# Optimization experiments

Hardware: AMD Instinct MI355X
Metric: run time of the kernel (lower is better)

## Reference

```python
import jax, jax.numpy as jnp
import numpy as np

EMBED = 256
HID = EMBED * 4
NUM_EXPERTS = 4
WINDOW = 16
B, T = 4, 4096
EPS = 1e-5


def _ln(x, g, b):
    m = jnp.mean(x, axis=-1, keepdims=True)
    v = jnp.mean(jnp.square(x - m), axis=-1, keepdims=True)
    return (x - m) / jnp.sqrt(v + EPS) * g + b


def setup_inputs() -> dict:
    key = jax.random.key(0)
    ks = jax.random.split(key, 16)
    s = 0.02
    d = {
        'x': jax.random.normal(ks[0], (B, T, EMBED), jnp.float32),
        'ln1_g': jnp.ones((EMBED,), jnp.float32),
        'ln1_b': jnp.zeros((EMBED,), jnp.float32),
        'qkv_w': jax.random.normal(ks[1], (EMBED, 3 * EMBED), jnp.float32) * s,
        'qkv_b': jnp.zeros((3 * EMBED,), jnp.float32),
        'proj_w': jax.random.normal(ks[2], (EMBED, EMBED), jnp.float32) * s,
        'proj_b': jnp.zeros((EMBED,), jnp.float32),
        'attn_gate': jnp.ones((EMBED,), jnp.float32),
        'ln2_g': jnp.ones((EMBED,), jnp.float32),
        'ln2_b': jnp.zeros((EMBED,), jnp.float32),
        'gating_w': jax.random.normal(ks[3], (EMBED, NUM_EXPERTS), jnp.float32) * s,
        'gating_b': jnp.zeros((NUM_EXPERTS,), jnp.float32),
        'e_w1': jax.random.normal(ks[4], (NUM_EXPERTS, EMBED, HID), jnp.float32) * s,
        'e_b1': jnp.zeros((NUM_EXPERTS, HID), jnp.float32),
        'e_w2': jax.random.normal(ks[5], (NUM_EXPERTS, HID, EMBED), jnp.float32) * s,
        'e_b2': jnp.zeros((NUM_EXPERTS, EMBED), jnp.float32),
    }
    return d


def reference(x, ln1_g, ln1_b, qkv_w, qkv_b, proj_w, proj_b, attn_gate,
              ln2_g, ln2_b, gating_w, gating_b, e_w1, e_b1, e_w2, e_b2):
    Bx, Tx, C = x.shape
    # --- sparse attention branch ---
    h = _ln(x, ln1_g, ln1_b)
    qkv = h @ qkv_w + qkv_b                      # [B,T,3C]
    q, k, v = jnp.split(qkv, 3, axis=-1)
    scores = jnp.einsum('btc,bsc->bts', q, k) / jnp.sqrt(jnp.float32(C))
    idx = jnp.arange(Tx)
    diff = idx[:, None] - idx[None, :]           # i - j
    in_window = (diff >= 0) & (diff <= WINDOW)
    # faithful to torch code: scores outside the window (but causal) stay 0,
    # positions above the diagonal become -inf; softmax over full row
    scores = jnp.where(in_window, scores, 0.0)
    scores = jnp.where(diff >= 0, scores, -jnp.inf)
    att = jax.nn.softmax(scores, axis=-1)        # [B,T,T]
    a_out = jnp.einsum('bts,bsc->btc', att, v) * attn_gate
    x = x + a_out @ proj_w + proj_b
    # --- dense all-expert MoE branch ---
    h2 = _ln(x, ln2_g, ln2_b)
    gates = jax.nn.softmax(h2 @ gating_w + gating_b, axis=-1)     # [B,T,E]
    hid = jax.nn.gelu(jnp.einsum('btc,ech->bteh', h2, e_w1) + e_b1,
                      approximate=False)                           # [B,T,E,H]
    eo = jnp.einsum('bteh,eho->bteo', hid, e_w2) + e_b2            # [B,T,E,C]
    moe_out = jnp.einsum('bte,bteo->bto', gates, eo)
    return x + moe_out
```

## Files before the change

### kernel.cpp

```cpp
#include <hip/hip_runtime.h>
#include <hip/hip_bf16.h>
#include <math.h>

#define T_   4096
#define B_   4
#define C_   256
#define C3_  768
#define H_   1024
#define E_   4
#define M_   (B_*T_)
#define NCH_ 64
#define CHL_ (T_/NCH_)

typedef __attribute__((ext_vector_type(8))) short short8;
typedef __attribute__((ext_vector_type(4))) float floatx4;

__device__ __forceinline__ float b2f(unsigned short u) {
  union { unsigned int i; float f; } x; x.i = ((unsigned int)u) << 16; return x.f;
}
__device__ __forceinline__ unsigned short f2b(float f) {
  __hip_bfloat16 h = __float2bfloat16(f);
  return *reinterpret_cast<unsigned short*>(&h);
}
__device__ __forceinline__ void unpack8(uint4 a, float* f) {
  unsigned int w[4] = {a.x, a.y, a.z, a.w};
  #pragma unroll
  for (int i = 0; i < 4; i++) {
    union { unsigned int u; float g; } lo, hi;
    lo.u = w[i] << 16; hi.u = w[i] & 0xffff0000u;
    f[2*i] = lo.g; f[2*i+1] = hi.g;
  }
}
__device__ __forceinline__ void gl_lds16(const unsigned short* g, unsigned short* l) {
  __builtin_amdgcn_global_load_lds(
      (const __attribute__((address_space(1))) void*)g,
      (__attribute__((address_space(3))) void*)l, 16, 0, 0);
}
__device__ __forceinline__ float gelu_f(float v) {
  float s = v * 0.70710678118f;
  float a = fabsf(s);
  float t = __builtin_amdgcn_rcpf(1.0f + 0.47047f * a);
  float poly = t * (0.3480242f + t * (-0.0958798f + t * 0.7478556f));
  float e = __expf(-a * a);
  float erfa = 1.0f - poly * e;
  float erfv = (s >= 0.f) ? erfa : -erfa;
  return 0.5f * v * (1.0f + erfv);
}

__global__ __launch_bounds__(256) void transpose_cvt(
    const float* __restrict__ src, unsigned short* __restrict__ dst, int K, int N,
    int dstLd, size_t dstZStride) {
  __shared__ float tile[32][33];
  src += (size_t)blockIdx.z * K * N;
  dst += (size_t)blockIdx.z * dstZStride;
  int n0 = blockIdx.x * 32, k0 = blockIdx.y * 32;
  int tx = threadIdx.x, ty = threadIdx.y;
  #pragma unroll
  for (int i = 0; i < 32; i += 8)
    tile[ty + i][tx] = src[(size_t)(k0 + ty + i) * N + n0 + tx];
  __syncthreads();
  #pragma unroll
  for (int i = 0; i < 32; i += 8)
    dst[(size_t)(n0 + ty + i) * dstLd + k0 + tx] = f2b(tile[tx][ty + i]);
}

__global__ __launch_bounds__(256) void ln1_kernel(
    const float* __restrict__ x, const float* __restrict__ g,
    const float* __restrict__ b, unsigned short* __restrict__ h) {
  __shared__ float red[4];
  int row = blockIdx.x, tid = threadIdx.x;
  float v = x[(size_t)row * C_ + tid];
  float s = v;
  #pragma unroll
  for (int o = 32; o; o >>= 1) s += __shfl_xor(s, o);
  if ((tid & 63) == 0) red[tid >> 6] = s;
  __syncthreads();
  float mean = (red[0] + red[1] + red[2] + red[3]) * (1.0f / C_);
  __syncthreads();
  float d = v - mean;
  float q = d * d;
  #pragma unroll
  for (int o = 32; o; o >>= 1) q += __shfl_xor(q, o);
  if ((tid & 63) == 0) red[tid >> 6] = q;
  __syncthreads();
  float var = (red[0] + red[1] + red[2] + red[3]) * (1.0f / C_);
  h[(size_t)row * C_ + tid] = f2b(d * rsqrtf(var + 1e-5f) * g[tid] + b[tid]);
}

__global__ __launch_bounds__(256) void ln2_gates_kernel(
    const float* __restrict__ x1, const float* __restrict__ g,
    const float* __restrict__ b, const float* __restrict__ gw,
    const float* __restrict__ gb, unsigned short* __restrict__ h2,
    float* __restrict__ gates) {
  __shared__ float red[4];
  __shared__ float redg[4][4];
  int row = blockIdx.x, tid = threadIdx.x;
  float v = x1[(size_t)row * C_ + tid];
  float s = v;
  #pragma unroll
  for (int o = 32; o; o >>= 1) s += __shfl_xor(s, o);
  if ((tid & 63) == 0) red[tid >> 6] = s;
  __syncthreads();
  float mean = (red[0] + red[1] + red[2] + red[3]) * (1.0f / C_);
  __syncthreads();
  float d = v - mean;
  float q = d * d;
  #pragma unroll
  for (int o = 32; o; o >>= 1) q += __shfl_xor(q, o);
  if ((tid & 63) == 0) red[tid >> 6] = q;
  __syncthreads();
  float var = (red[0] + red[1] + red[2] + red[3]) * (1.0f / C_);
  float hv = d * rsqrtf(var + 1e-5f) * g[tid] + b[tid];
  h2[(size_t)row * C_ + tid] = f2b(hv);
  float p0 = hv * gw[tid * 4 + 0];
  float p1 = hv * gw[tid * 4 + 1];
  float p2 = hv * gw[tid * 4 + 2];
  float p3 = hv * gw[tid * 4 + 3];
  #pragma unroll
  for (int o = 32; o; o >>= 1) {
    p0 += __shfl_xor(p0, o); p1 += __shfl_xor(p1, o);
    p2 += __shfl_xor(p2, o); p3 += __shfl_xor(p3, o);
  }
  if ((tid & 63) == 0) {
    int w = tid >> 6;
    redg[w][0] = p0; redg[w][1] = p1; redg[w][2] = p2; redg[w][3] = p3;
  }
  __syncthreads();
  if (tid == 0) {
    float t4[4];
    #pragma unroll
    for (int e = 0; e < 4; e++)
      t4[e] = redg[0][e] + redg[1][e] + redg[2][e] + redg[3][e] + gb[e];
    float m = fmaxf(fmaxf(t4[0], t4[1]), fmaxf(t4[2], t4[3]));
    float zs = 0.f;
    #pragma unroll
    for (int e = 0; e < 4; e++) { t4[e] = __expf(t4[e] - m); zs += t4[e]; }
    float inv = 1.0f / zs;
    #pragma unroll
    for (int e = 0; e < 4; e++) gates[(size_t)row * 4 + e] = t4[e] * inv;
  }
}

__global__ __launch_bounds__(256) void scan1_kernel(const unsigned short* __restrict__ qkv,
                                                    float* __restrict__ S) {
  int b = blockIdx.x >> 6, ch = blockIdx.x & 63, c = threadIdx.x;
  float s = 0.f;
  size_t base = ((size_t)b * T_ + (size_t)ch * CHL_) * C3_ + 512 + c;
  for (int t = 0; t < CHL_; t++) s += b2f(qkv[base + (size_t)t * C3_]);
  S[((size_t)b * NCH_ + ch) * C_ + c] = s;
}
__global__ __launch_bounds__(256) void scan2_kernel(float* __restrict__ S) {
  int b = blockIdx.x, c = threadIdx.x;
  float run = 0.f;
  for (int ch = 0; ch < NCH_; ch++) {
    size_t i = ((size_t)b * NCH_ + ch) * C_ + c;
    float t = S[i]; S[i] = run; run += t;
  }
}
__global__ __launch_bounds__(256) void scan3_kernel(const unsigned short* __restrict__ qkv,
                                                    const float* __restrict__ S,
                                                    unsigned short* __restrict__ Pb) {
  int b = blockIdx.x >> 6, ch = blockIdx.x & 63, c = threadIdx.x;
  float run = S[((size_t)b * NCH_ + ch) * C_ + c];
  size_t row0 = (size_t)b * T_ + (size_t)ch * CHL_;
  for (int t = 0; t < CHL_; t++) {
    run += b2f(qkv[(row0 + t) * C3_ + 512 + c]);
    Pb[(row0 + t) * C_ + c] = f2b(run);
  }
}

__global__ __launch_bounds__(256) void attn_kernel(
    const unsigned short* __restrict__ qkv, const unsigned short* __restrict__ Pb,
    const float* __restrict__ gate, unsigned short* __restrict__ aout) {
  int wave = threadIdx.x >> 6, lane = threadIdx.x & 63;
  int r = blockIdx.x * 4 + wave;
  int t = r & (T_ - 1);
  int g = lane >> 4, u = lane & 15;
  const unsigned short* qp = qkv + (size_t)r * C3_ + (u << 4);
  float qv[16];
  unpack8(*(const uint4*)qp, qv);
  unpack8(*(const uint4*)(qp + 8), qv + 8);
  float sc[5];
  #pragma unroll
  for (int rnd = 0; rnd < 5; rnd++) {
    int j = rnd * 4 + g;
    int jj = t - 16 + j;
    bool valid = (j <= 16) && (jj >= 0);
    float d = 0.f;
    if (valid) {
      const unsigned short* kp = qkv + (size_t)(r - 16 + j) * C3_ + 256 + (u << 4);
      float kv[16];
      unpack8(*(const uint4*)kp, kv);
      unpack8(*(const uint4*)(kp + 8), kv + 8);
      #pragma unroll
      for (int c = 0; c < 16; c++) d += qv[c] * kv[c];
    }
    d += __shfl_xor(d, 1); d += __shfl_xor(d, 2);
    d += __shfl_xor(d, 4); d += __shfl_xor(d, 8);
    sc[rnd] = valid ? d * 0.0625f : -1e30f;
  }
  float m = fmaxf(fmaxf(fmaxf(sc[0], sc[1]), fmaxf(sc[2], sc[3])), sc[4]);
  m = fmaxf(m, __shfl_xor(m, 16));
  m = fmaxf(m, __shfl_xor(m, 32));
  if (t > 16) m = fmaxf(m, 0.0f);
  float ev[5], Zp = 0.f;
  #pragma unroll
  for (int rnd = 0; rnd < 5; rnd++) {
    ev[rnd] = (sc[rnd] > -1e29f) ? __expf(sc[rnd] - m) : 0.f;
    Zp += ev[rnd];
  }
  Zp += __shfl_xor(Zp, 16);
  Zp += __shfl_xor(Zp, 32);
  float e0v = 0.f;
  if (t > 16) { e0v = __expf(-m); Zp += e0v * (float)(t - 16); }
  float vp[16];
  #pragma unroll
  for (int c = 0; c < 16; c++) vp[c] = 0.f;
  #pragma unroll
  for (int rnd = 0; rnd < 5; rnd++) {
    if (ev[rnd] != 0.f) {
      int j = rnd * 4 + g;
      const unsigned short* vpp = qkv + (size_t)(r - 16 + j) * C3_ + 512 + (u << 4);
      float vv[16];
      unpack8(*(const uint4*)vpp, vv);
      unpack8(*(const uint4*)(vpp + 8), vv + 8);
      #pragma unroll
      for (int c = 0; c < 16; c++) vp[c] += ev[rnd] * vv[c];
    }
  }
  #pragma unroll
  for (int c = 0; c < 16; c++) {
    vp[c] += __shfl_xor(vp[c], 16);
    vp[c] += __shfl_xor(vp[c], 32);
  }
  if (g == 0) {
    if (t > 16) {
      const unsigned short* pp = Pb + (size_t)(r - 17) * C_ + (u << 4);
      float pv[16];
      unpack8(*(const uint4*)pp, pv);
      unpack8(*(const uint4*)(pp + 8), pv + 8);
      #pragma unroll
      for (int c = 0; c < 16; c++) vp[c] += e0v * pv[c];
    }
    float inv = 1.0f / Zp;
    const float* gp = gate + (u << 4);
    unsigned int ow[8];
    #pragma unroll
    for (int i = 0; i < 8; i++) {
      unsigned short lo = f2b(vp[2*i] * inv * gp[2*i]);
      unsigned short hi = f2b(vp[2*i+1] * inv * gp[2*i+1]);
      ow[i] = (unsigned int)lo | ((unsigned int)hi << 16);
    }
    uint4 s0 = {ow[0], ow[1], ow[2], ow[3]};
    uint4 s1 = {ow[4], ow[5], ow[6], ow[7]};
    *(uint4*)(aout + (size_t)r * C_ + (u << 4)) = s0;
    *(uint4*)(aout + (size_t)r * C_ + (u << 4) + 8) = s1;
  }
}

template<int EPI>
__global__ __launch_bounds__(256) void gemm128(
    const unsigned short* __restrict__ A, const unsigned short* __restrict__ Bt,
    const float* __restrict__ bias, int K, int ldOut,
    const float* __restrict__ resid, float* __restrict__ outf,
    unsigned short* __restrict__ outb, const float* __restrict__ gates) {
  __shared__ __align__(16) unsigned short As[128 * 64];
  __shared__ __align__(16) unsigned short Bs[128 * 64];
  const int tid = threadIdx.x;
  const int wave = tid >> 6, lane = tid & 63;
  const int mBlk = blockIdx.x * 128, nBlk = blockIdx.y * 128;
  const int wm = (wave >> 1) * 64, wn = (wave & 1) * 64;
  const int lm = lane & 15, lk = (lane >> 4) * 8;
  floatx4 acc[4][4];
  #pragma unroll
  for (int i = 0; i < 4; i++)
    #pragma unroll
    for (int j = 0; j < 4; j++) acc[i][j] = (floatx4){0.f, 0.f, 0.f, 0.f};

  for (int kt = 0; kt < K; kt += 64) {
    __syncthreads();
    #pragma unroll
    for (int i = 0; i < 4; i++) {
      int seg = i * 256 + tid;
      int row = seg >> 3, g = seg & 7;
      int gc = (g ^ (row & 7)) << 3;
      gl_lds16(A + (size_t)(mBlk + row) * K + kt + gc, &As[seg * 8]);
      gl_lds16(Bt + (size_t)(nBlk + row) * K + kt + gc, &Bs[seg * 8]);
    }
    __syncthreads();
    #pragma unroll
    for (int kk = 0; kk < 64; kk += 32) {
      short8 mf[4], nf[4];
      #pragma unroll
      for (int j = 0; j < 4; j++) {
        int row = wm + j * 16 + lm;
        mf[j] = *(const short8*)&As[row * 64 + ((((kk + lk) >> 3) ^ (row & 7)) << 3)];
      }
      #pragma unroll
      for (int i = 0; i < 4; i++) {
        int row = wn + i * 16 + lm;
        nf[i] = *(const short8*)&Bs[row * 64 + ((((kk + lk) >> 3) ^ (row & 7)) << 3)];
      }
      #pragma unroll
      for (int i = 0; i < 4; i++)
        #pragma unroll
        for (int j = 0; j < 4; j++)
          acc[i][j] = __builtin_amdgcn_mfma_f32_16x16x32_bf16(nf[i], mf[j], acc[i][j], 0, 0, 0);
    }
  }
  const int lc = lane & 15, q4 = (lane >> 4) * 4;
  const int eIdx = (EPI == 2) ? (nBlk >> 10) : 0;
  #pragma unroll
  for (int i = 0; i < 4; i++) {
    int n0 = nBlk + wn + i * 16 + q4;
    float4 bs = *(const float4*)&bias[n0];
    #pragma unroll
    for (int j = 0; j < 4; j++) {
      int m = mBlk + wm + j * 16 + lc;
      float v0 = acc[i][j][0] + bs.x, v1 = acc[i][j][1] + bs.y;
      float v2 = acc[i][j][2] + bs.z, v3 = acc[i][j][3] + bs.w;
      if (EPI == 0) {
        ushort4 o = {f2b(v0), f2b(v1), f2b(v2), f2b(v3)};
        *(ushort4*)&outb[(size_t)m * ldOut + n0] = o;
      } else if (EPI == 1) {
        size_t idx = (size_t)m * ldOut + n0;
        float4 r = *(const float4*)&resid[idx];
        float4 o = {v0 + r.x, v1 + r.y, v2 + r.z, v3 + r.w};
        *(float4*)&outf[idx] = o;
      } else {
        float g = gates[(size_t)m * E_ + eIdx];
        ushort4 o = {f2b(g * gelu_f(v0)), f2b(g * gelu_f(v1)),
                     f2b(g * gelu_f(v2)), f2b(g * gelu_f(v3))};
        *(ushort4*)&outb[(size_t)m * ldOut + n0] = o;
      }
    }
  }
}

__global__ __launch_bounds__(256) void gemm_down(
    const unsigned short* __restrict__ hid, const unsigned short* __restrict__ w2cat,
    const float* __restrict__ b2, const float* __restrict__ gates,
    const float* __restrict__ x1, float* __restrict__ out) {
  __shared__ __align__(16) unsigned short As[128 * 64];
  __shared__ __align__(16) unsigned short Bs[64 * 64];
  const int tid = threadIdx.x;
  const int wave = tid >> 6, lane = tid & 63;
  const int mBlk = blockIdx.x * 128, nBlk = blockIdx.y * 64;
  const int wm = wave * 32;
  const int lm = lane & 15, lk = (lane >> 4) * 8;
  floatx4 acc[4][2];
  #pragma unroll
  for (int i = 0; i < 4; i++)
    #pragma unroll
    for (int j = 0; j < 2; j++) acc[i][j] = (floatx4){0.f, 0.f, 0.f, 0.f};

  const int K = E_ * H_;
  for (int kt = 0; kt < K; kt += 64) {
    __syncthreads();
    #pragma unroll
    for (int i = 0; i < 4; i++) {
      int seg = i * 256 + tid;
      int row = seg >> 3, g = seg & 7;
      int gc = (g ^ (row & 7)) << 3;
      gl_lds16(hid + (size_t)(mBlk + row) * K + kt + gc, &As[seg * 8]);
    }
    #pragma unroll
    for (int i = 0; i < 2; i++) {
      int seg = i * 256 + tid;
      int row = seg >> 3, g = seg & 7;
      int gc = (g ^ (row & 7)) << 3;
      gl_lds16(w2cat + (size_t)(nBlk + row) * K + kt + gc, &Bs[seg * 8]);
    }
    __syncthreads();
    #pragma unroll
    for (int kk = 0; kk < 64; kk += 32) {
      short8 mf[2], nf[4];
      #pragma unroll
      for (int j = 0; j < 2; j++) {
        int row = wm + j * 16 + lm;
        mf[j] = *(const short8*)&As[row * 64 + ((((kk + lk) >> 3) ^ (row & 7)) << 3)];
      }
      #pragma unroll
      for (int i = 0; i < 4; i++) {
        int row = i * 16 + lm;
        nf[i] = *(const short8*)&Bs[row * 64 + ((((kk + lk) >> 3) ^ (row & 7)) << 3)];
      }
      #pragma unroll
      for (int i = 0; i < 4; i++)
        #pragma unroll
        for (int j = 0; j < 2; j++)
          acc[i][j] = __builtin_amdgcn_mfma_f32_16x16x32_bf16(nf[i], mf[j], acc[i][j], 0, 0, 0);
    }
  }
  const int lc = lane & 15, q4 = (lane >> 4) * 4;
  #pragma unroll
  for (int j = 0; j < 2; j++) {
    int m = mBlk + wm + j * 16 + lc;
    float4 g4 = *(const float4*)(gates + (size_t)m * 4);
    #pragma unroll
    for (int i = 0; i < 4; i++) {
      int n0 = nBlk + i * 16 + q4;
      float4 bA = *(const float4*)&b2[0 * C_ + n0];
      float4 bB = *(const float4*)&b2[1 * C_ + n0];
      float4 bC = *(const float4*)&b2[2 * C_ + n0];
      float4 bD = *(const float4*)&b2[3 * C_ + n0];
      size_t idx = (size_t)m * C_ + n0;
      float4 r = *(const float4*)&x1[idx];
      float4 o;
      o.x = acc[i][j][0] + r.x + g4.x*bA.x + g4.y*bB.x + g4.z*bC.x + g4.w*bD.x;
      o.y = acc[i][j][1] + r.y + g4.x*bA.y + g4.y*bB.y + g4.z*bC.y + g4.w*bD.y;
      o.z = acc[i][j][2] + r.z + g4.x*bA.z + g4.y*bB.z + g4.z*bC.z + g4.w*bD.z;
      o.w = acc[i][j][3] + r.w + g4.x*bA.w + g4.y*bB.w + g4.z*bC.w + g4.w*bD.w;
      *(float4*)&out[idx] = o;
    }
  }
}

extern "C" void kernel_launch(void* const* d_in, const int* in_sizes, int n_in,
                              void* d_out, int out_size, void* d_ws, size_t ws_size,
                              hipStream_t stream) {
  const float* x       = (const float*)d_in[0];
  const float* ln1_g   = (const float*)d_in[1];
  const float* ln1_b   = (const float*)d_in[2];
  const float* qkv_w   = (const float*)d_in[3];
  const float* qkv_b   = (const float*)d_in[4];
  const float* proj_w  = (const float*)d_in[5];
  const float* proj_b  = (const float*)d_in[6];
  const float* attn_g  = (const float*)d_in[7];
  const float* ln2_g   = (const float*)d_in[8];
  const float* ln2_b   = (const float*)d_in[9];
  const float* gat_w   = (const float*)d_in[10];
  const float* gat_b   = (const float*)d_in[11];
  const float* e_w1    = (const float*)d_in[12];
  const float* e_b1    = (const float*)d_in[13];
  const float* e_w2    = (const float*)d_in[14];
  const float* e_b2    = (const float*)d_in[15];
  float* out = (float*)d_out;

  char* p = (char*)d_ws;
  unsigned short* h    = (unsigned short*)p; p += (size_t)M_ * C_ * 2;
  unsigned short* qkv  = (unsigned short*)p; p += (size_t)M_ * C3_ * 2;
  unsigned short* Pb   = (unsigned short*)p; p += (size_t)M_ * C_ * 2;
  unsigned short* aout = (unsigned short*)p; p += (size_t)M_ * C_ * 2;
  float*          x1   = (float*)p;          p += (size_t)M_ * C_ * 4;
  unsigned short* h2   = (unsigned short*)p; p += (size_t)M_ * C_ * 2;
  float*          gts  = (float*)p;          p += (size_t)M_ * E_ * 4;
  float*          S    = (float*)p;          p += (size_t)B_ * NCH_ * C_ * 4;
  unsigned short* wq   = (unsigned short*)p; p += (size_t)C3_ * C_ * 2;
  unsigned short* wp   = (unsigned short*)p; p += (size_t)C_ * C_ * 2;
  unsigned short* w1t  = (unsigned short*)p; p += (size_t)E_ * H_ * C_ * 2;
  unsigned short* w2t  = (unsigned short*)p; p += (size_t)E_ * C_ * H_ * 2;
  unsigned short* hid  = (unsigned short*)p; p += (size_t)M_ * E_ * H_ * 2;

  dim3 t32x8(32, 8);
  transpose_cvt<<<dim3(C3_/32, C_/32, 1), t32x8, 0, stream>>>(qkv_w, wq, C_, C3_, C_, 0);
  transpose_cvt<<<dim3(C_/32, C_/32, 1),  t32x8, 0, stream>>>(proj_w, wp, C_, C_, C_, 0);
  transpose_cvt<<<dim3(H_/32, C_/32, E_), t32x8, 0, stream>>>(e_w1, w1t, C_, H_, C_, (size_t)H_ * C_);
  transpose_cvt<<<dim3(C_/32, H_/32, E_), t32x8, 0, stream>>>(e_w2, w2t, H_, C_, E_ * H_, (size_t)H_);

  ln1_kernel<<<M_, 256, 0, stream>>>(x, ln1_g, ln1_b, h);
  gemm128<0><<<dim3(M_/128, C3_/128), 256, 0, stream>>>(h, wq, qkv_b, C_, C3_,
      nullptr, nullptr, qkv, nullptr);
  scan1_kernel<<<B_*NCH_, 256, 0, stream>>>(qkv, S);
  scan2_kernel<<<B_, 256, 0, stream>>>(S);
  scan3_kernel<<<B_*NCH_, 256, 0, stream>>>(qkv, S, Pb);
  attn_kernel<<<M_/4, 256, 0, stream>>>(qkv, Pb, attn_g, aout);
  gemm128<1><<<dim3(M_/128, C_/128), 256, 0, stream>>>(aout, wp, proj_b, C_, C_,
      x, x1, nullptr, nullptr);
  ln2_gates_kernel<<<M_, 256, 0, stream>>>(x1, ln2_g, ln2_b, gat_w, gat_b, h2, gts);
  gemm128<2><<<dim3(M_/128, (E_*H_)/128), 256, 0, stream>>>(h2, w1t, e_b1, C_, E_ * H_,
      nullptr, nullptr, hid, gts);
  gemm_down<<<dim3(M_/128, C_/64), 256, 0, stream>>>(hid, w2t, e_b2, gts, x1, out);
}
```

Baseline: 373.6 us.

## Fuse MoE up and down projections into one kernel with split-expert partials

```diff
diff --git a/kernel.cpp b/kernel.cpp
--- a/kernel.cpp
+++ b/kernel.cpp
@@ -263,7 +263,7 @@
     const unsigned short* __restrict__ A, const unsigned short* __restrict__ Bt,
     const float* __restrict__ bias, int K, int ldOut,
     const float* __restrict__ resid, float* __restrict__ outf,
-    unsigned short* __restrict__ outb, const float* __restrict__ gates) {
+    unsigned short* __restrict__ outb) {
   __shared__ __align__(16) unsigned short As[128 * 64];
   __shared__ __align__(16) unsigned short Bs[128 * 64];
   const int tid = threadIdx.x;
@@ -309,7 +309,6 @@
     }
   }
   const int lc = lane & 15, q4 = (lane >> 4) * 4;
-  const int eIdx = (EPI == 2) ? (nBlk >> 10) : 0;
   #pragma unroll
   for (int i = 0; i < 4; i++) {
     int n0 = nBlk + wn + i * 16 + q4;
@@ -322,98 +321,140 @@
       if (EPI == 0) {
         ushort4 o = {f2b(v0), f2b(v1), f2b(v2), f2b(v3)};
         *(ushort4*)&outb[(size_t)m * ldOut + n0] = o;
-      } else if (EPI == 1) {
+      } else {
         size_t idx = (size_t)m * ldOut + n0;
         float4 r = *(const float4*)&resid[idx];
         float4 o = {v0 + r.x, v1 + r.y, v2 + r.z, v3 + r.w};
         *(float4*)&outf[idx] = o;
-      } else {
-        float g = gates[(size_t)m * E_ + eIdx];
-        ushort4 o = {f2b(g * gelu_f(v0)), f2b(g * gelu_f(v1)),
-                     f2b(g * gelu_f(v2)), f2b(g * gelu_f(v3))};
-        *(ushort4*)&outb[(size_t)m * ldOut + n0] = o;
       }
     }
   }
 }
 
-__global__ __launch_bounds__(256) void gemm_down(
-    const unsigned short* __restrict__ hid, const unsigned short* __restrict__ w2cat,
+__global__ __launch_bounds__(512, 2) void moe_fused(
+    const unsigned short* __restrict__ h2, const unsigned short* __restrict__ w1t,
+    const unsigned short* __restrict__ w2cat, const float* __restrict__ b1,
     const float* __restrict__ b2, const float* __restrict__ gates,
-    const float* __restrict__ x1, float* __restrict__ out) {
-  __shared__ __align__(16) unsigned short As[128 * 64];
-  __shared__ __align__(16) unsigned short Bs[64 * 64];
-  const int tid = threadIdx.x;
-  const int wave = tid >> 6, lane = tid & 63;
-  const int mBlk = blockIdx.x * 128, nBlk = blockIdx.y * 64;
-  const int wm = wave * 32;
-  const int lm = lane & 15, lk = (lane >> 4) * 8;
-  floatx4 acc[4][2];
+    const float* __restrict__ x1, float* __restrict__ part) {
+  __shared__ __align__(16) unsigned short w1b[2][32 * 256];
+  __shared__ __align__(16) unsigned short Pl[128 * 40];
+  const int tid = threadIdx.x, wave = tid >> 6, lane = tid & 63;
+  const int lm = lane & 15, quad = lane >> 4, q4 = quad * 4, lk = quad * 8;
+  const int mBlk = blockIdx.x * 128;
+  const int z = blockIdx.y, e0 = z * 2;
+  const int wm = (wave >> 2) * 64, wn = (wave & 3) * 64;
+  const int m1 = wave * 16 + lm;
+
+  const float g1a = gates[(size_t)(mBlk + m1) * 4 + e0];
+  const float g1b = gates[(size_t)(mBlk + m1) * 4 + e0 + 1];
+
+  short8 acache[8];
+  #pragma unroll
+  for (int ks = 0; ks < 8; ks++)
+    acache[ks] = *(const short8*)(h2 + (size_t)(mBlk + m1) * C_ + ks * 32 + lk);
+
+  floatx4 oacc[4][4];
   #pragma unroll
   for (int i = 0; i < 4; i++)
     #pragma unroll
-    for (int j = 0; j < 2; j++) acc[i][j] = (floatx4){0.f, 0.f, 0.f, 0.f};
-
-  const int K = E_ * H_;
-  for (int kt = 0; kt < K; kt += 64) {
+    for (int j = 0; j < 4; j++) oacc[i][j] = (floatx4){0.f, 0.f, 0.f, 0.f};
+
+  auto stage = [&](int ch, int buf) {
+    int e = e0 + (ch >> 5), hc = (ch & 31) * 32;
+    const unsigned short* w1src = w1t + ((size_t)e * H_ + hc) * C_;
+    #pragma unroll
+    for (int i = 0; i < 2; i++) {
+      int seg = i * 512 + tid;
+      int row = seg >> 5, s = seg & 31;
+      int sp = (s & 24) | ((s & 7) ^ (row & 7));
+      gl_lds16(w1src + (size_t)row * C_ + sp * 8, &w1b[buf][seg * 8]);
+    }
+  };
+
+  stage(0, 0);
+  __syncthreads();
+
+  #pragma unroll 1
+  for (int ch = 0; ch < 64; ch++) {
+    const int buf = ch & 1;
+    const int e = e0 + (ch >> 5), hc = (ch & 31) * 32;
+    short8 w2f[4];
+    #pragma unroll
+    for (int i = 0; i < 4; i++)
+      w2f[i] = *(const short8*)(w2cat + (size_t)(wn + i * 16 + lm) * (E_ * H_) +
+                                (size_t)e * H_ + hc + lk);
+    if (ch + 1 < 64) stage(ch + 1, buf ^ 1);
+    floatx4 pacc[2];
+    pacc[0] = (floatx4){0.f, 0.f, 0.f, 0.f};
+    pacc[1] = (floatx4){0.f, 0.f, 0.f, 0.f};
+    #pragma unroll
+    for (int ks = 0; ks < 8; ks++) {
+      int s = ks * 4 + quad;
+      #pragma unroll
+      for (int j = 0; j < 2; j++) {
+        int row = j * 16 + lm;
+        int sp = (s & 24) | ((s & 7) ^ (row & 7));
+        short8 nf = *(const short8*)&w1b[buf][row * 256 + sp * 8];
+        pacc[j] = __builtin_amdgcn_mfma_f32_16x16x32_bf16(nf, acache[ks], pacc[j], 0, 0, 0);
+      }
+    }
     __syncthreads();
+    const float ge = (ch >> 5) ? g1b : g1a;
+    #pragma unroll
+    for (int j = 0; j < 2; j++) {
+      float4 bb = *(const float4*)&b1[(size_t)e * H_ + hc + j * 16 + q4];
+      ushort4 o;
+      o.x = f2b(ge * gelu_f(pacc[j][0] + bb.x));
+      o.y = f2b(ge * gelu_f(pacc[j][1] + bb.y));
+      o.z = f2b(ge * gelu_f(pacc[j][2] + bb.z));
+      o.w = f2b(ge * gelu_f(pacc[j][3] + bb.w));
+      *(ushort4*)&Pl[m1 * 40 + j * 16 + q4] = o;
+    }
+    __syncthreads();
+    short8 mf[4];
+    #pragma unroll
+    for (int j = 0; j < 4; j++)
+      mf[j] = *(const short8*)&Pl[(wm + j * 16 + lm) * 40 + lk];
+    #pragma unroll
+    for (int i = 0; i < 4; i++)
+      #pragma unroll
+      for (int j = 0; j < 4; j++)
+        oacc[i][j] = __builtin_amdgcn_mfma_f32_16x16x32_bf16(w2f[i], mf[j], oacc[i][j], 0, 0, 0);
+  }
+  #pragma unroll
+  for (int j = 0; j < 4; j++) {
+    int m = mBlk + wm + j * 16 + lm;
+    float ga = gates[(size_t)m * 4 + e0];
+    float gb = gates[(size_t)m * 4 + e0 + 1];
     #pragma unroll
     for (int i = 0; i < 4; i++) {
-      int seg = i * 256 + tid;
-      int row = seg >> 3, g = seg & 7;
-      int gc = (g ^ (row & 7)) << 3;
-      gl_lds16(hid + (size_t)(mBlk + row) * K + kt + gc, &As[seg * 8]);
-    }
-    #pragma unroll
-    for (int i = 0; i < 2; i++) {
-      int seg = i * 256 + tid;
-      int row = seg >> 3, g = seg & 7;
-      int gc = (g ^ (row & 7)) << 3;
-      gl_lds16(w2cat + (size_t)(nBlk + row) * K + kt + gc, &Bs[seg * 8]);
-    }
-    __syncthreads();
-    #pragma unroll
-    for (int kk = 0; kk < 64; kk += 32) {
-      short8 mf[2], nf[4];
-      #pragma unroll
-      for (int j = 0; j < 2; j++) {
-        int row = wm + j * 16 + lm;
-        mf[j] = *(const short8*)&As[row * 64 + ((((kk + lk) >> 3) ^ (row & 7)) << 3)];
+      int n0 = wn + i * 16 + q4;
+      float4 bA = *(const float4*)&b2[(size_t)e0 * C_ + n0];
+      float4 bB = *(const float4*)&b2[(size_t)(e0 + 1) * C_ + n0];
+      size_t idx = (size_t)m * C_ + n0;
+      float4 o;
+      o.x = oacc[i][j][0] + ga * bA.x + gb * bB.x;
+      o.y = oacc[i][j][1] + ga * bA.y + gb * bB.y;
+      o.z = oacc[i][j][2] + ga * bA.z + gb * bB.z;
+      o.w = oacc[i][j][3] + ga * bA.w + gb * bB.w;
+      if (z == 0) {
+        float4 r = *(const float4*)&x1[idx];
+        o.x += r.x; o.y += r.y; o.z += r.z; o.w += r.w;
       }
-      #pragma unroll
-      for (int i = 0; i < 4; i++) {
-        int row = i * 16 + lm;
-        nf[i] = *(const short8*)&Bs[row * 64 + ((((kk + lk) >> 3) ^ (row & 7)) << 3)];
-      }
-      #pragma unroll
-      for (int i = 0; i < 4; i++)
-        #pragma unroll
-        for (int j = 0; j < 2; j++)
-          acc[i][j] = __builtin_amdgcn_mfma_f32_16x16x32_bf16(nf[i], mf[j], acc[i][j], 0, 0, 0);
-    }
-  }
-  const int lc = lane & 15, q4 = (lane >> 4) * 4;
-  #pragma unroll
-  for (int j = 0; j < 2; j++) {
-    int m = mBlk + wm + j * 16 + lc;
-    float4 g4 = *(const float4*)(gates + (size_t)m * 4);
-    #pragma unroll
-    for (int i = 0; i < 4; i++) {
-      int n0 = nBlk + i * 16 + q4;
-      float4 bA = *(const float4*)&b2[0 * C_ + n0];
-      float4 bB = *(const float4*)&b2[1 * C_ + n0];
-      float4 bC = *(const float4*)&b2[2 * C_ + n0];
-      float4 bD = *(const float4*)&b2[3 * C_ + n0];
-      size_t idx = (size_t)m * C_ + n0;
-      float4 r = *(const float4*)&x1[idx];
-      float4 o;
-      o.x = acc[i][j][0] + r.x + g4.x*bA.x + g4.y*bB.x + g4.z*bC.x + g4.w*bD.x;
-      o.y = acc[i][j][1] + r.y + g4.x*bA.y + g4.y*bB.y + g4.z*bC.y + g4.w*bD.y;
-      o.z = acc[i][j][2] + r.z + g4.x*bA.z + g4.y*bB.z + g4.z*bC.z + g4.w*bD.z;
-      o.w = acc[i][j][3] + r.w + g4.x*bA.w + g4.y*bB.w + g4.z*bC.w + g4.w*bD.w;
-      *(float4*)&out[idx] = o;
-    }
-  }
+      *(float4*)&part[(size_t)z * M_ * C_ + idx] = o;
+    }
+  }
+}
+
+__global__ __launch_bounds__(256) void combine_kernel(
+    float* __restrict__ out, const float* __restrict__ part) {
+  size_t i = ((size_t)blockIdx.x * 256 + threadIdx.x);
+  const float4* p0 = (const float4*)part;
+  const float4* p1 = (const float4*)(part + (size_t)M_ * C_);
+  float4* o = (float4*)out;
+  float4 u = p0[i], v = p1[i];
+  float4 a = {u.x + v.x, u.y + v.y, u.z + v.z, u.w + v.w};
+  o[i] = a;
 }
 
 extern "C" void kernel_launch(void* const* d_in, const int* in_sizes, int n_in,
@@ -450,7 +491,7 @@
   unsigned short* wp   = (unsigned short*)p; p += (size_t)C_ * C_ * 2;
   unsigned short* w1t  = (unsigned short*)p; p += (size_t)E_ * H_ * C_ * 2;
   unsigned short* w2t  = (unsigned short*)p; p += (size_t)E_ * C_ * H_ * 2;
-  unsigned short* hid  = (unsigned short*)p; p += (size_t)M_ * E_ * H_ * 2;
+  float*          part = (float*)p;          p += (size_t)2 * M_ * C_ * 4;
 
   dim3 t32x8(32, 8);
   transpose_cvt<<<dim3(C3_/32, C_/32, 1), t32x8, 0, stream>>>(qkv_w, wq, C_, C3_, C_, 0);
@@ -460,15 +501,14 @@
 
   ln1_kernel<<<M_, 256, 0, stream>>>(x, ln1_g, ln1_b, h);
   gemm128<0><<<dim3(M_/128, C3_/128), 256, 0, stream>>>(h, wq, qkv_b, C_, C3_,
-      nullptr, nullptr, qkv, nullptr);
+      nullptr, nullptr, qkv);
   scan1_kernel<<<B_*NCH_, 256, 0, stream>>>(qkv, S);
   scan2_kernel<<<B_, 256, 0, stream>>>(S);
   scan3_kernel<<<B_*NCH_, 256, 0, stream>>>(qkv, S, Pb);
   attn_kernel<<<M_/4, 256, 0, stream>>>(qkv, Pb, attn_g, aout);
   gemm128<1><<<dim3(M_/128, C_/128), 256, 0, stream>>>(aout, wp, proj_b, C_, C_,
-      x, x1, nullptr, nullptr);
+      x, x1, nullptr);
   ln2_gates_kernel<<<M_, 256, 0, stream>>>(x1, ln2_g, ln2_b, gat_w, gat_b, h2, gts);
-  gemm128<2><<<dim3(M_/128, (E_*H_)/128), 256, 0, stream>>>(h2, w1t, e_b1, C_, E_ * H_,
-      nullptr, nullptr, hid, gts);
-  gemm_down<<<dim3(M_/128, C_/64), 256, 0, stream>>>(hid, w2t, e_b2, gts, x1, out);
-}
+  moe_fused<<<dim3(M_/128, 2), 512, 0, stream>>>(h2, w1t, w2t, e_b1, e_b2, gts, x1, part);
+  combine_kernel<<<(M_*C_)/(256*4), 256, 0, stream>>>(out, part);
+}
```

New measurement: 389.2 us. +4.2%, slower.

## Store MoE hidden activations and W2 in fp8 and use fp8 MFMA for down-projection

Applied to the files above, without the earlier changes.

```diff
diff --git a/kernel.cpp b/kernel.cpp
--- a/kernel.cpp
+++ b/kernel.cpp
@@ -11,6 +11,7 @@
 #define M_   (B_*T_)
 #define NCH_ 64
 #define CHL_ (T_/NCH_)
+#define KH_  4096
 
 typedef __attribute__((ext_vector_type(8))) short short8;
 typedef __attribute__((ext_vector_type(4))) float floatx4;
@@ -31,7 +32,7 @@
     f[2*i] = lo.g; f[2*i+1] = hi.g;
   }
 }
-__device__ __forceinline__ void gl_lds16(const unsigned short* g, unsigned short* l) {
+__device__ __forceinline__ void gl_lds16(const void* g, void* l) {
   __builtin_amdgcn_global_load_lds(
       (const __attribute__((address_space(1))) void*)g,
       (__attribute__((address_space(3))) void*)l, 16, 0, 0);
@@ -46,6 +47,12 @@
   float erfv = (s >= 0.f) ? erfa : -erfa;
   return 0.5f * v * (1.0f + erfv);
 }
+__device__ __forceinline__ unsigned int pk_fp8x4(float a, float b, float c, float d) {
+  unsigned int v = 0;
+  v = __builtin_amdgcn_cvt_pk_fp8_f32(a, b, v, false);
+  v = __builtin_amdgcn_cvt_pk_fp8_f32(c, d, v, true);
+  return v;
+}
 
 __global__ __launch_bounds__(256) void transpose_cvt(
     const float* __restrict__ src, unsigned short* __restrict__ dst, int K, int N,
@@ -62,6 +69,27 @@
   #pragma unroll
   for (int i = 0; i < 32; i += 8)
     dst[(size_t)(n0 + ty + i) * dstLd + k0 + tx] = f2b(tile[tx][ty + i]);
+}
+
+__global__ __launch_bounds__(256) void transpose_w2_fp8(
+    const float* __restrict__ src, unsigned char* __restrict__ dst) {
+  __shared__ float tile[32][33];
+  int e = blockIdx.z;
+  src += (size_t)e * H_ * C_;
+  int h0 = blockIdx.x * 32, c0 = blockIdx.y * 32;
+  int tx = threadIdx.x, ty = threadIdx.y;
+  #pragma unroll
+  for (int i = 0; i < 32; i += 8)
+    tile[ty + i][tx] = src[(size_t)(h0 + ty + i) * C_ + c0 + tx];
+  __syncthreads();
+  int k = e * H_ + h0 + tx;
+  int kp = (k & ~63) | ((k & 48) >> 2) | ((k & 12) << 2) | (k & 3);
+  #pragma unroll
+  for (int i = 0; i < 32; i += 8) {
+    float v = tile[tx][ty + i] * 256.0f;
+    dst[(size_t)(c0 + ty + i) * KH_ + kp] =
+        (unsigned char)(__builtin_amdgcn_cvt_pk_fp8_f32(v, v, 0, false) & 0xff);
+  }
 }
 
 __global__ __launch_bounds__(256) void ln1_kernel(
@@ -263,7 +291,8 @@
     const unsigned short* __restrict__ A, const unsigned short* __restrict__ Bt,
     const float* __restrict__ bias, int K, int ldOut,
     const float* __restrict__ resid, float* __restrict__ outf,
-    unsigned short* __restrict__ outb, const float* __restrict__ gates) {
+    unsigned short* __restrict__ outb, unsigned char* __restrict__ outf8,
+    const float* __restrict__ gates) {
   __shared__ __align__(16) unsigned short As[128 * 64];
   __shared__ __align__(16) unsigned short Bs[128 * 64];
   const int tid = threadIdx.x;
@@ -308,94 +337,111 @@
           acc[i][j] = __builtin_amdgcn_mfma_f32_16x16x32_bf16(nf[i], mf[j], acc[i][j], 0, 0, 0);
     }
   }
-  const int lc = lane & 15, q4 = (lane >> 4) * 4;
-  const int eIdx = (EPI == 2) ? (nBlk >> 10) : 0;
-  #pragma unroll
-  for (int i = 0; i < 4; i++) {
-    int n0 = nBlk + wn + i * 16 + q4;
-    float4 bs = *(const float4*)&bias[n0];
+  const int lc = lane & 15, quad = lane >> 4, q4 = quad * 4;
+  if (EPI == 2) {
+    const int eIdx = nBlk >> 10;
     #pragma unroll
     for (int j = 0; j < 4; j++) {
       int m = mBlk + wm + j * 16 + lc;
-      float v0 = acc[i][j][0] + bs.x, v1 = acc[i][j][1] + bs.y;
-      float v2 = acc[i][j][2] + bs.z, v3 = acc[i][j][3] + bs.w;
-      if (EPI == 0) {
-        ushort4 o = {f2b(v0), f2b(v1), f2b(v2), f2b(v3)};
-        *(ushort4*)&outb[(size_t)m * ldOut + n0] = o;
-      } else if (EPI == 1) {
-        size_t idx = (size_t)m * ldOut + n0;
-        float4 r = *(const float4*)&resid[idx];
-        float4 o = {v0 + r.x, v1 + r.y, v2 + r.z, v3 + r.w};
-        *(float4*)&outf[idx] = o;
-      } else {
-        float g = gates[(size_t)m * E_ + eIdx];
-        ushort4 o = {f2b(g * gelu_f(v0)), f2b(g * gelu_f(v1)),
-                     f2b(g * gelu_f(v2)), f2b(g * gelu_f(v3))};
-        *(ushort4*)&outb[(size_t)m * ldOut + n0] = o;
+      float gs = 64.0f * gates[(size_t)m * E_ + eIdx];
+      unsigned int w[4];
+      #pragma unroll
+      for (int i = 0; i < 4; i++) {
+        int n0 = nBlk + wn + i * 16 + q4;
+        float4 bs = *(const float4*)&bias[n0];
+        w[i] = pk_fp8x4(gs * gelu_f(acc[i][j][0] + bs.x),
+                        gs * gelu_f(acc[i][j][1] + bs.y),
+                        gs * gelu_f(acc[i][j][2] + bs.z),
+                        gs * gelu_f(acc[i][j][3] + bs.w));
       }
+      uint4 st = {w[0], w[1], w[2], w[3]};
+      *(uint4*)&outf8[(size_t)m * KH_ + nBlk + wn + quad * 16] = st;
+    }
+  } else {
+    #pragma unroll
+    for (int i = 0; i < 4; i++) {
+      int n0 = nBlk + wn + i * 16 + q4;
+      float4 bs = *(const float4*)&bias[n0];
+      #pragma unroll
+      for (int j = 0; j < 4; j++) {
+        int m = mBlk + wm + j * 16 + lc;
+        float v0 = acc[i][j][0] + bs.x, v1 = acc[i][j][1] + bs.y;
+        float v2 = acc[i][j][2] + bs.z, v3 = acc[i][j][3] + bs.w;
+        if (EPI == 0) {
+          ushort4 o = {f2b(v0), f2b(v1), f2b(v2), f2b(v3)};
+          *(ushort4*)&outb[(size_t)m * ldOut + n0] = o;
+        } else {
+          size_t idx = (size_t)m * ldOut + n0;
+          float4 r = *(const float4*)&resid[idx];
+          float4 o = {v0 + r.x, v1 + r.y, v2 + r.z, v3 + r.w};
+          *(float4*)&outf[idx] = o;
+        }
+      }
     }
   }
 }
 
 __global__ __launch_bounds__(256) void gemm_down(
-    const unsigned short* __restrict__ hid, const unsigned short* __restrict__ w2cat,
+    const unsigned char* __restrict__ hid8, const unsigned char* __restrict__ w2f8,
     const float* __restrict__ b2, const float* __restrict__ gates,
     const float* __restrict__ x1, float* __restrict__ out) {
-  __shared__ __align__(16) unsigned short As[128 * 64];
-  __shared__ __align__(16) unsigned short Bs[64 * 64];
+  __shared__ __align__(16) unsigned char As[128 * 128];
+  __shared__ __align__(16) unsigned char Bs[64 * 128];
   const int tid = threadIdx.x;
   const int wave = tid >> 6, lane = tid & 63;
   const int mBlk = blockIdx.x * 128, nBlk = blockIdx.y * 64;
   const int wm = wave * 32;
-  const int lm = lane & 15, lk = (lane >> 4) * 8;
+  const int lm = lane & 15, quad = lane >> 4;
   floatx4 acc[4][2];
   #pragma unroll
   for (int i = 0; i < 4; i++)
     #pragma unroll
     for (int j = 0; j < 2; j++) acc[i][j] = (floatx4){0.f, 0.f, 0.f, 0.f};
 
-  const int K = E_ * H_;
-  for (int kt = 0; kt < K; kt += 64) {
+  for (int kt = 0; kt < KH_; kt += 128) {
     __syncthreads();
     #pragma unroll
-    for (int i = 0; i < 4; i++) {
-      int seg = i * 256 + tid;
-      int row = seg >> 3, g = seg & 7;
-      int gc = (g ^ (row & 7)) << 3;
-      gl_lds16(hid + (size_t)(mBlk + row) * K + kt + gc, &As[seg * 8]);
-    }
-    #pragma unroll
-    for (int i = 0; i < 2; i++) {
-      int seg = i * 256 + tid;
-      int row = seg >> 3, g = seg & 7;
-      int gc = (g ^ (row & 7)) << 3;
-      gl_lds16(w2cat + (size_t)(nBlk + row) * K + kt + gc, &Bs[seg * 8]);
+    for (int r = 0; r < 4; r++) {
+      int seg = r * 256 + tid;
+      int row = seg >> 3, s = seg & 7;
+      int sp = s ^ (row & 7);
+      gl_lds16(hid8 + (size_t)(mBlk + row) * KH_ + kt + sp * 16, &As[seg * 16]);
+    }
+    #pragma unroll
+    for (int r = 0; r < 2; r++) {
+      int seg = r * 256 + tid;
+      int row = seg >> 3, s = seg & 7;
+      int sp = s ^ (row & 7);
+      gl_lds16(w2f8 + (size_t)(nBlk + row) * KH_ + kt + sp * 16, &Bs[seg * 16]);
     }
     __syncthreads();
     #pragma unroll
-    for (int kk = 0; kk < 64; kk += 32) {
-      short8 mf[2], nf[4];
+    for (int kk = 0; kk < 4; kk++) {
+      int c8 = kk * 4 + quad;
+      int s = c8 >> 1, h8 = (c8 & 1) * 8;
+      long mf[2], nf[4];
       #pragma unroll
       for (int j = 0; j < 2; j++) {
         int row = wm + j * 16 + lm;
-        mf[j] = *(const short8*)&As[row * 64 + ((((kk + lk) >> 3) ^ (row & 7)) << 3)];
+        mf[j] = *(const long*)&As[row * 128 + ((s ^ (row & 7)) << 4) + h8];
       }
       #pragma unroll
       for (int i = 0; i < 4; i++) {
         int row = i * 16 + lm;
-        nf[i] = *(const short8*)&Bs[row * 64 + ((((kk + lk) >> 3) ^ (row & 7)) << 3)];
+        nf[i] = *(const long*)&Bs[row * 128 + ((s ^ (row & 7)) << 4) + h8];
       }
       #pragma unroll
       for (int i = 0; i < 4; i++)
         #pragma unroll
         for (int j = 0; j < 2; j++)
-          acc[i][j] = __builtin_amdgcn_mfma_f32_16x16x32_bf16(nf[i], mf[j], acc[i][j], 0, 0, 0);
-    }
-  }
-  const int lc = lane & 15, q4 = (lane >> 4) * 4;
+          acc[i][j] = __builtin_amdgcn_mfma_f32_16x16x32_fp8_fp8(nf[i], mf[j], acc[i][j], 0, 0, 0);
+    }
+  }
+  const float sc = 1.0f / 16384.0f;
+  const int q4 = quad * 4;
   #pragma unroll
   for (int j = 0; j < 2; j++) {
-    int m = mBlk + wm + j * 16 + lc;
+    int m = mBlk + wm + j * 16 + lm;
     float4 g4 = *(const float4*)(gates + (size_t)m * 4);
     #pragma unroll
     for (int i = 0; i < 4; i++) {
@@ -407,10 +453,10 @@
       size_t idx = (size_t)m * C_ + n0;
       float4 r = *(const float4*)&x1[idx];
       float4 o;
-      o.x = acc[i][j][0] + r.x + g4.x*bA.x + g4.y*bB.x + g4.z*bC.x + g4.w*bD.x;
-      o.y = acc[i][j][1] + r.y + g4.x*bA.y + g4.y*bB.y + g4.z*bC.y + g4.w*bD.y;
-      o.z = acc[i][j][2] + r.z + g4.x*bA.z + g4.y*bB.z + g4.z*bC.z + g4.w*bD.z;
-      o.w = acc[i][j][3] + r.w + g4.x*bA.w + g4.y*bB.w + g4.z*bC.w + g4.w*bD.w;
+      o.x = acc[i][j][0]*sc + r.x + g4.x*bA.x + g4.y*bB.x + g4.z*bC.x + g4.w*bD.x;
+      o.y = acc[i][j][1]*sc + r.y + g4.x*bA.y + g4.y*bB.y + g4.z*bC.y + g4.w*bD.y;
+      o.z = acc[i][j][2]*sc + r.z + g4.x*bA.z + g4.y*bB.z + g4.z*bC.z + g4.w*bD.z;
+      o.w = acc[i][j][3]*sc + r.w + g4.x*bA.w + g4.y*bB.w + g4.z*bC.w + g4.w*bD.w;
       *(float4*)&out[idx] = o;
     }
   }
@@ -449,26 +495,26 @@
   unsigned short* wq   = (unsigned short*)p; p += (size_t)C3_ * C_ * 2;
   unsigned short* wp   = (unsigned short*)p; p += (size_t)C_ * C_ * 2;
   unsigned short* w1t  = (unsigned short*)p; p += (size_t)E_ * H_ * C_ * 2;
-  unsigned short* w2t  = (unsigned short*)p; p += (size_t)E_ * C_ * H_ * 2;
-  unsigned short* hid  = (unsigned short*)p; p += (size_t)M_ * E_ * H_ * 2;
+  unsigned char*  w2f8 = (unsigned char*)p;  p += (size_t)C_ * KH_;
+  unsigned char*  hid8 = (unsigned char*)p;  p += (size_t)M_ * KH_;
 
   dim3 t32x8(32, 8);
   transpose_cvt<<<dim3(C3_/32, C_/32, 1), t32x8, 0, stream>>>(qkv_w, wq, C_, C3_, C_, 0);
   transpose_cvt<<<dim3(C_/32, C_/32, 1),  t32x8, 0, stream>>>(proj_w, wp, C_, C_, C_, 0);
   transpose_cvt<<<dim3(H_/32, C_/32, E_), t32x8, 0, stream>>>(e_w1, w1t, C_, H_, C_, (size_t)H_ * C_);
-  transpose_cvt<<<dim3(C_/32, H_/32, E_), t32x8, 0, stream>>>(e_w2, w2t, H_, C_, E_ * H_, (size_t)H_);
+  transpose_w2_fp8<<<dim3(H_/32, C_/32, E_), t32x8, 0, stream>>>(e_w2, w2f8);
 
   ln1_kernel<<<M_, 256, 0, stream>>>(x, ln1_g, ln1_b, h);
   gemm128<0><<<dim3(M_/128, C3_/128), 256, 0, stream>>>(h, wq, qkv_b, C_, C3_,
-      nullptr, nullptr, qkv, nullptr);
+      nullptr, nullptr, qkv, nullptr, nullptr);
   scan1_kernel<<<B_*NCH_, 256, 0, stream>>>(qkv, S);
   scan2_kernel<<<B_, 256, 0, stream>>>(S);
   scan3_kernel<<<B_*NCH_, 256, 0, stream>>>(qkv, S, Pb);
   attn_kernel<<<M_/4, 256, 0, stream>>>(qkv, Pb, attn_g, aout);
   gemm128<1><<<dim3(M_/128, C_/128), 256, 0, stream>>>(aout, wp, proj_b, C_, C_,
-      x, x1, nullptr, nullptr);
+      x, x1, nullptr, nullptr, nullptr);
   ln2_gates_kernel<<<M_, 256, 0, stream>>>(x1, ln2_g, ln2_b, gat_w, gat_b, h2, gts);
-  gemm128<2><<<dim3(M_/128, (E_*H_)/128), 256, 0, stream>>>(h2, w1t, e_b1, C_, E_ * H_,
-      nullptr, nullptr, hid, gts);
-  gemm_down<<<dim3(M_/128, C_/64), 256, 0, stream>>>(hid, w2t, e_b2, gts, x1, out);
-}
+  gemm128<2><<<dim3(M_/128, KH_/128), 256, 0, stream>>>(h2, w1t, e_b1, C_, 0,
+      nullptr, nullptr, nullptr, hid8, gts);
+  gemm_down<<<dim3(M_/128, C_/64), 256, 0, stream>>>(hid8, w2f8, e_b2, gts, x1, out);
+}
```

Result: faster. 330.1 us (-11.6%).
